# Optimization experiments

Measured on AMD Instinct MI355X. Metric: run time of the kernel, lower is better.

Reference implementation:

```python
import jax, jax.numpy as jnp
import numpy as np
from jax import lax

B, L = 16, 256
NUM_ITEMS, NUM_ATTRS = 30000, 2000
D_MODEL, D_STATE, D_CONV, N_LAYERS = 256, 16, 4, 4
D_INNER = 2 * D_MODEL
DT_RANK = (D_MODEL + 15) // 16  # ceil(d_model/16)
LN_EPS = 1e-5


def setup_inputs() -> dict:
    key = jax.random.key(0)
    ks = jax.random.split(key, 12)
    def nrm(k, shape, scale):
        return jax.random.normal(k, shape, jnp.float32) * scale
    inp = {}
    inp["seq"] = jax.random.randint(ks[0], (B, L), 0, NUM_ITEMS)
    inp["attr"] = jax.random.randint(ks[1], (B, L), 0, NUM_ATTRS)
    inp["item_emb"] = nrm(ks[2], (NUM_ITEMS, D_MODEL), 0.02)
    inp["attr_emb"] = nrm(ks[3], (NUM_ATTRS, D_MODEL), 0.02)
    inp["alpha"] = jnp.float32(0.5)
    inp["ln_s"] = jnp.ones((D_MODEL,), jnp.float32)
    inp["ln_b"] = jnp.zeros((D_MODEL,), jnp.float32)
    inp["in_w"] = nrm(ks[4], (N_LAYERS, D_MODEL, 2 * D_INNER), D_MODEL ** -0.5)
    inp["conv_w"] = nrm(ks[5], (N_LAYERS, D_INNER, 1, D_CONV), D_CONV ** -0.5)  # depthwise OIH
    inp["conv_b"] = jnp.zeros((N_LAYERS, D_INNER), jnp.float32)
    inp["xp_w"] = nrm(ks[6], (N_LAYERS, D_INNER, DT_RANK + 2 * D_STATE), D_INNER ** -0.5)
    inp["dt_w"] = nrm(ks[7], (N_LAYERS, DT_RANK, D_INNER), DT_RANK ** -0.5)
    inp["dt_b"] = jnp.zeros((N_LAYERS, D_INNER), jnp.float32)
    inp["A_log"] = jnp.tile(jnp.log(jnp.arange(1, D_STATE + 1, dtype=jnp.float32)), (N_LAYERS, D_INNER, 1))
    inp["D_p"] = jnp.ones((N_LAYERS, D_INNER), jnp.float32)
    inp["out_w"] = nrm(ks[8], (N_LAYERS, D_INNER, D_MODEL), D_INNER ** -0.5)
    inp["nrm_s"] = jnp.ones((N_LAYERS, D_MODEL), jnp.float32)
    inp["nrm_b"] = jnp.zeros((N_LAYERS, D_MODEL), jnp.float32)
    inp["head_w"] = nrm(ks[9], (D_MODEL, NUM_ITEMS), D_MODEL ** -0.5)
    return inp


def _silu(x):
    return x * jax.nn.sigmoid(x)


def _layernorm(x, s, b):
    m = jnp.mean(x, axis=-1, keepdims=True)
    v = jnp.mean(jnp.square(x - m), axis=-1, keepdims=True)
    return (x - m) * lax.rsqrt(v + LN_EPS) * s + b


def _holo_bind(x, y):
    # circular convolution via orthonormal rFFT
    xf = jnp.fft.rfft(x, axis=-1, norm="ortho")
    yf = jnp.fft.rfft(y, axis=-1, norm="ortho")
    return jnp.fft.irfft(xf * yf, n=x.shape[-1], axis=-1, norm="ortho")


def _mamba(x, in_w, conv_w, conv_b, xp_w, dt_w, dt_b, A_log, D_p, out_w):
    # x: [B, L, D_MODEL]
    xi, z = jnp.split(x @ in_w, 2, axis=-1)  # each [B, L, D_INNER]
    # causal depthwise conv (torch pads both sides then truncates to L == left pad)
    xc = lax.conv_general_dilated(
        xi.transpose(0, 2, 1), conv_w, (1,), [(D_CONV - 1, 0)],
        feature_group_count=D_INNER, dimension_numbers=("NCH", "OIH", "NCH"),
    ) + conv_b[None, :, None]
    xc = _silu(xc).transpose(0, 2, 1)  # [B, L, D_INNER]
    dt, B_ssm, C_ssm = jnp.split(xc @ xp_w, [DT_RANK, DT_RANK + D_STATE], axis=-1)
    dt = jax.nn.softplus(dt @ dt_w + dt_b)  # [B, L, D_INNER]
    A = -jnp.exp(A_log)  # [D_INNER, D_STATE]
    dA = jnp.exp(jnp.einsum("bld,dn->bldn", dt, A))
    dBx = jnp.einsum("bld,bln->bldn", dt, B_ssm) * xc[..., None]

    def step(h, inp):
        dA_t, dBx_t, C_t = inp
        h = dA_t * h + dBx_t  # [B, D_INNER, D_STATE]
        return h, jnp.einsum("bdn,bn->bd", h, C_t)

    h0 = jnp.zeros((x.shape[0], D_INNER, D_STATE), x.dtype)
    _, ys = lax.scan(step, h0, (dA.transpose(1, 0, 2, 3), dBx.transpose(1, 0, 2, 3), C_ssm.transpose(1, 0, 2)))
    y = ys.transpose(1, 0, 2) + xc * D_p
    return (y * _silu(z)) @ out_w


def reference(seq, attr, item_emb, attr_emb, alpha, ln_s, ln_b, in_w, conv_w, conv_b,
              xp_w, dt_w, dt_b, A_log, D_p, out_w, nrm_s, nrm_b, head_w):
    ie = item_emb.at[0].set(0.0)  # padding_idx=0
    ae = attr_emb.at[0].set(0.0)
    ei, ea = ie[seq], ae[attr]  # [B, L, D_MODEL]
    x = _layernorm(ei + alpha * _holo_bind(ei, ea), ln_s, ln_b)
    for l in range(N_LAYERS):
        x = x + _mamba(_layernorm(x, nrm_s[l], nrm_b[l]), in_w[l], conv_w[l], conv_b[l],
                       xp_w[l], dt_w[l], dt_b[l], A_log[l], D_p[l], out_w[l])
    return x @ head_w  # [B, L, NUM_ITEMS]
```

## Files before the change

kernel.cpp:

```cpp
#include <hip/hip_runtime.h>
#include <hip/hip_bf16.h>
#include <math.h>

#define BB 16
#define LL 256
#define DM 256
#define DI 512
#define DS 16
#define DTR 16
#define NTOK (BB*LL)
#define LN_EPS 1e-5f

typedef __attribute__((ext_vector_type(8))) short bf16x8;
typedef __attribute__((ext_vector_type(4))) float f32x4;
typedef __attribute__((ext_vector_type(4))) unsigned int u32x4;

__device__ __forceinline__ float siluf(float x) { return x / (1.f + expf(-x)); }

__device__ __forceinline__ unsigned short f2bf(float f) {
    union { float f; unsigned int u; } x; x.f = f;
    unsigned int r = x.u + 0x7fffu + ((x.u >> 16) & 1u);
    return (unsigned short)(r >> 16);
}
__device__ __forceinline__ float bf2f(unsigned short h) {
    union { unsigned int u; float f; } x; x.u = ((unsigned int)h) << 16; return x.f;
}

__device__ __forceinline__ void block_reduce2(float& s, float& s2, float* red) {
    #pragma unroll
    for (int off = 32; off; off >>= 1) {
        s  += __shfl_down(s,  off);
        s2 += __shfl_down(s2, off);
    }
    int wid = threadIdx.x >> 6;
    if ((threadIdx.x & 63) == 0) { red[wid*2] = s; red[wid*2+1] = s2; }
    __syncthreads();
    s  = red[0] + red[2] + red[4] + red[6];
    s2 = red[1] + red[3] + red[5] + red[7];
}

__global__ __launch_bounds__(256)
void embed_holo_ln(const int* __restrict__ seq, const int* __restrict__ attr,
                   const float* __restrict__ item_emb, const float* __restrict__ attr_emb,
                   const float* __restrict__ alpha_p, const float* __restrict__ ln_s,
                   const float* __restrict__ ln_b, float* __restrict__ x) {
    int t = blockIdx.x;
    int k = threadIdx.x;
    __shared__ float ei[DM], ea[DM];
    __shared__ float red[8];
    int si = seq[t], ai = attr[t];
    ei[k] = (si == 0) ? 0.f : item_emb[(size_t)si * DM + k];
    ea[k] = (ai == 0) ? 0.f : attr_emb[(size_t)ai * DM + k];
    __syncthreads();
    float c0 = 0.f, c1 = 0.f, c2 = 0.f, c3 = 0.f;
    #pragma unroll 8
    for (int j = 0; j < DM; j += 4) {
        c0 = fmaf(ei[j],   ea[(k - j)     & 255], c0);
        c1 = fmaf(ei[j+1], ea[(k - j - 1) & 255], c1);
        c2 = fmaf(ei[j+2], ea[(k - j - 2) & 255], c2);
        c3 = fmaf(ei[j+3], ea[(k - j - 3) & 255], c3);
    }
    float conv = (c0 + c1) + (c2 + c3);
    float v = fmaf(alpha_p[0] * 0.0625f, conv, ei[k]);
    float s = v, s2 = v * v;
    block_reduce2(s, s2, red);
    float m  = s * (1.f / DM);
    float var = s2 * (1.f / DM) - m * m;
    x[(size_t)t * DM + k] = (v - m) * rsqrtf(var + LN_EPS) * ln_s[k] + ln_b[k];
}

__global__ __launch_bounds__(256)
void ln_split2(const float* __restrict__ in, const float* __restrict__ sc,
               const float* __restrict__ bi, unsigned short* __restrict__ Ap) {
    int t = blockIdx.x, k = threadIdx.x;
    __shared__ float red[8];
    float v = in[(size_t)t * DM + k];
    float s = v, s2 = v * v;
    block_reduce2(s, s2, red);
    float m  = s * (1.f / DM);
    float var = s2 * (1.f / DM) - m * m;
    float o = (v - m) * rsqrtf(var + LN_EPS) * sc[k] + bi[k];
    unsigned short hi = f2bf(o);
    size_t base = (size_t)t * (2 * DM);
    Ap[base + k] = hi; Ap[base + DM + k] = hi;
}

__global__ __launch_bounds__(256)
void cvt_B2(const float* __restrict__ W, unsigned short* __restrict__ Bt, int K, int N) {
    int k0 = blockIdx.x * 64, n0 = blockIdx.y * 64;
    int K2 = 2 * K;
    __shared__ float tile[64][65];
    int tid = threadIdx.x;
    #pragma unroll
    for (int i = 0; i < 16; ++i) {
        int idx = tid + i * 256;
        int r = idx >> 6, c = idx & 63;
        int n = n0 + c;
        tile[r][c] = (n < N) ? W[(size_t)(k0 + r) * N + n] : 0.f;
    }
    __syncthreads();
    int nn = tid >> 2, kb = (tid & 3) * 16;
    alignas(16) unsigned short hv[16], lv[16];
    #pragma unroll
    for (int j = 0; j < 16; ++j) {
        float v = tile[kb + j][nn];
        hv[j] = f2bf(v); lv[j] = f2bf(v - bf2f(hv[j]));
    }
    size_t base = (size_t)(n0 + nn) * K2 + k0 + kb;
    *(u32x4*)&Bt[base]         = *(u32x4*)&hv[0];
    *(u32x4*)&Bt[base + 8]     = *(u32x4*)&hv[8];
    *(u32x4*)&Bt[base + K]     = *(u32x4*)&lv[0];
    *(u32x4*)&Bt[base + K + 8] = *(u32x4*)&lv[8];
}

__global__ __launch_bounds__(256)
void cvt_B3(const float* __restrict__ W, unsigned short* __restrict__ Bt, int K, int N) {
    int k0 = blockIdx.x * 64, n0 = blockIdx.y * 64;
    int K3 = 3 * K;
    __shared__ float tile[64][65];
    int tid = threadIdx.x;
    #pragma unroll
    for (int i = 0; i < 16; ++i) {
        int idx = tid + i * 256;
        int r = idx >> 6, c = idx & 63;
        int n = n0 + c;
        tile[r][c] = (n < N) ? W[(size_t)(k0 + r) * N + n] : 0.f;
    }
    __syncthreads();
    int nn = tid >> 2, kb = (tid & 3) * 16;
    alignas(16) unsigned short hv[16], lv[16];
    #pragma unroll
    for (int j = 0; j < 16; ++j) {
        float v = tile[kb + j][nn];
        hv[j] = f2bf(v); lv[j] = f2bf(v - bf2f(hv[j]));
    }
    size_t base = (size_t)(n0 + nn) * K3 + k0 + kb;
    *(u32x4*)&Bt[base]           = *(u32x4*)&hv[0];
    *(u32x4*)&Bt[base + 8]       = *(u32x4*)&hv[8];
    *(u32x4*)&Bt[base + K]       = *(u32x4*)&lv[0];
    *(u32x4*)&Bt[base + K + 8]   = *(u32x4*)&lv[8];
    *(u32x4*)&Bt[base + 2*K]     = *(u32x4*)&hv[0];
    *(u32x4*)&Bt[base + 2*K + 8] = *(u32x4*)&hv[8];
}

__global__ __launch_bounds__(256)
void cvt_A3(const float* __restrict__ X, unsigned short* __restrict__ Ap) {
    int i = blockIdx.x * 256 + threadIdx.x;
    int t = i >> 5, kc = (i & 31) * 8;
    const float4* X4 = (const float4*)X;
    float4 v0 = X4[(size_t)i * 2], v1 = X4[(size_t)i * 2 + 1];
    float vv[8] = { v0.x, v0.y, v0.z, v0.w, v1.x, v1.y, v1.z, v1.w };
    alignas(16) unsigned short hv[8], lv[8];
    #pragma unroll
    for (int j = 0; j < 8; ++j) { hv[j] = f2bf(vv[j]); lv[j] = f2bf(vv[j] - bf2f(hv[j])); }
    size_t base = (size_t)t * 768 + kc;
    *(u32x4*)&Ap[base]       = *(u32x4*)&hv[0];
    *(u32x4*)&Ap[base + 256] = *(u32x4*)&hv[0];
    *(u32x4*)&Ap[base + 512] = *(u32x4*)&lv[0];
}

template<bool ACC, bool SWZ>
__global__ __launch_bounds__(256)
void gemm_bf16t(const unsigned short* __restrict__ A, const unsigned short* __restrict__ Bt,
                float* __restrict__ C, int N, int K) {
    __shared__ unsigned short sA[128 * 32];
    __shared__ unsigned short sB[128 * 32];
    int tid = threadIdx.x, lane = tid & 63, w = tid >> 6;
    int wr = w >> 1, wc = w & 1;
    int row0, col0;
    if (SWZ) {
        int nwg = gridDim.x * gridDim.y;
        int chunk = nwg >> 3;
        int bid = blockIdx.y * gridDim.x + blockIdx.x;
        int idx = (bid & 7) * chunk + (bid >> 3);
        int rowt = idx % gridDim.y;
        int colt = idx / gridDim.y;
        row0 = rowt * 128; col0 = colt * 128;
    } else {
        row0 = blockIdx.y * 128; col0 = blockIdx.x * 128;
    }
    f32x4 acc[4][4] = {};
    int rA = lane >> 2;
    int kc = (lane & 3) * 8;
    for (int k0 = 0; k0 < K; k0 += 32) {
        #pragma unroll
        for (int i = 0; i < 2; ++i) {
            int rr = (w * 2 + i) * 16 + rA;
            const unsigned short* ga = A  + (size_t)(row0 + rr) * K + k0 + kc;
            const unsigned short* gb = Bt + (size_t)(col0 + rr) * K + k0 + kc;
            __builtin_amdgcn_global_load_lds(
                (const __attribute__((address_space(1))) unsigned int*)ga,
                (__attribute__((address_space(3))) unsigned int*)(sA + (w * 2 + i) * 512), 16, 0, 0);
            __builtin_amdgcn_global_load_lds(
                (const __attribute__((address_space(1))) unsigned int*)gb,
                (__attribute__((address_space(3))) unsigned int*)(sB + (w * 2 + i) * 512), 16, 0, 0);
        }
        __syncthreads();
        bf16x8 av[4], bv[4];
        #pragma unroll
        for (int m = 0; m < 4; ++m)
            av[m] = *(const bf16x8*)(sA + (wr * 64 + m * 16 + (lane & 15)) * 32 + (lane >> 4) * 8);
        #pragma unroll
        for (int n = 0; n < 4; ++n)
            bv[n] = *(const bf16x8*)(sB + (wc * 64 + n * 16 + (lane & 15)) * 32 + (lane >> 4) * 8);
        #pragma unroll
        for (int m = 0; m < 4; ++m)
            #pragma unroll
            for (int n = 0; n < 4; ++n)
                acc[m][n] = __builtin_amdgcn_mfma_f32_16x16x32_bf16(av[m], bv[n], acc[m][n], 0, 0, 0);
        __syncthreads();
    }
    #pragma unroll
    for (int m = 0; m < 4; ++m) {
        int rg = row0 + wr * 64 + m * 16 + (lane >> 4) * 4;
        #pragma unroll
        for (int n = 0; n < 4; ++n) {
            int cg = col0 + wc * 64 + n * 16 + (lane & 15);
            if (cg < N) {
                float* p = C + (size_t)rg * N + cg;
                #pragma unroll
                for (int r = 0; r < 4; ++r) {
                    if (ACC)      p[(size_t)r * N] += acc[m][n][r];
                    else if (SWZ) __builtin_nontemporal_store(acc[m][n][r], p + (size_t)r * N);
                    else          p[(size_t)r * N]  = acc[m][n][r];
                }
            }
        }
    }
}

__global__ __launch_bounds__(256)
void conv_silu(const float* __restrict__ xz, const float* __restrict__ w,
               const float* __restrict__ cb, float* __restrict__ xc,
               unsigned short* __restrict__ Xc3) {
    int t = blockIdx.x;
    int d = (blockIdx.y << 8) + threadIdx.x;
    int l = t & (LL - 1);
    float acc = cb[d];
    #pragma unroll
    for (int tt = 0; tt < 4; ++tt) {
        int ls = l - 3 + tt;
        if (ls >= 0) acc = fmaf(xz[(size_t)(t - 3 + tt) * (2 * DI) + d], w[d * 4 + tt], acc);
    }
    float v = siluf(acc);
    xc[(size_t)t * DI + d] = v;
    unsigned short hi = f2bf(v), lo = f2bf(v - bf2f(hi));
    size_t base = (size_t)t * (3 * DI);
    Xc3[base + d] = hi; Xc3[base + DI + d] = hi; Xc3[base + 2 * DI + d] = lo;
}

#define NCH 4
#define TCH 64
__global__ __launch_bounds__(256)
void scan_p1(const float* __restrict__ dtbc, const float* __restrict__ xc,
             const float* __restrict__ dt_w, const float* __restrict__ dt_b,
             const float* __restrict__ A_log, const float* __restrict__ D_p,
             float* __restrict__ y, float* __restrict__ Hend, float* __restrict__ Pb) {
    int d = blockIdx.x * 256 + threadIdx.x;
    int b = blockIdx.y, c = blockIdx.z;
    int t0 = b * LL + c * TCH;
    __shared__ float rs[TCH * 48];
    const float* src = dtbc + (size_t)t0 * 48;
    #pragma unroll
    for (int i = 0; i < 12; ++i) rs[threadIdx.x + i * 256] = src[threadIdx.x + i * 256];
    __syncthreads();
    float Av[DS], h[DS], P[DS], Wd[DTR];
    #pragma unroll
    for (int n = 0; n < DS; ++n) { Av[n] = -expf(A_log[d * DS + n]); h[n] = 0.f; P[n] = 1.f; }
    #pragma unroll
    for (int k = 0; k < DTR; ++k) Wd[k] = dt_w[k * DI + d];
    float bias = dt_b[d], Dv = D_p[d];
    for (int t = 0; t < TCH; ++t) {
        const float* r = rs + t * 48;
        float s = bias;
        #pragma unroll
        for (int k = 0; k < DTR; ++k) s = fmaf(r[k], Wd[k], s);
        float dt = (s > 20.f) ? s : log1pf(expf(s));
        float xv = xc[(size_t)(t0 + t) * DI + d];
        float dtx = dt * xv, acc = 0.f;
        #pragma unroll
        for (int n = 0; n < DS; ++n) {
            float dA = expf(dt * Av[n]);
            h[n] = fmaf(dA, h[n], dtx * r[DTR + n]);
            P[n] *= dA;
            acc = fmaf(h[n], r[DTR + DS + n], acc);
        }
        y[(size_t)(t0 + t) * DI + d] = fmaf(xv, Dv, acc);
    }
    size_t sb = ((size_t)(b * NCH + c) * DI + d) * DS;
    #pragma unroll
    for (int n = 0; n < DS; ++n) { Hend[sb + n] = h[n]; Pb[sb + n] = P[n]; }
}

__global__ __launch_bounds__(256)
void scan_p2(const float* __restrict__ dtbc,
             const float* __restrict__ dt_w, const float* __restrict__ dt_b,
             const float* __restrict__ A_log,
             float* __restrict__ y, const float* __restrict__ Hend,
             const float* __restrict__ Pb) {
    int d = blockIdx.x * 256 + threadIdx.x;
    int b = blockIdx.y, c = blockIdx.z + 1;
    int t0 = b * LL + c * TCH;
    __shared__ float rs[TCH * 48];
    const float* src = dtbc + (size_t)t0 * 48;
    #pragma unroll
    for (int i = 0; i < 12; ++i) rs[threadIdx.x + i * 256] = src[threadIdx.x + i * 256];
    __syncthreads();
    float Av[DS], g[DS], Wd[DTR];
    #pragma unroll
    for (int n = 0; n < DS; ++n) Av[n] = -expf(A_log[d * DS + n]);
    #pragma unroll
    for (int k = 0; k < DTR; ++k) Wd[k] = dt_w[k * DI + d];
    float bias = dt_b[d];
    {
        size_t sb0 = ((size_t)(b * NCH + 0) * DI + d) * DS;
        #pragma unroll
        for (int n = 0; n < DS; ++n) g[n] = Hend[sb0 + n];
        for (int cc = 1; cc < c; ++cc) {
            size_t sb = ((size_t)(b * NCH + cc) * DI + d) * DS;
            #pragma unroll
            for (int n = 0; n < DS; ++n) g[n] = fmaf(Pb[sb + n], g[n], Hend[sb + n]);
        }
    }
    for (int t = 0; t < TCH; ++t) {
        const float* r = rs + t * 48;
        float s = bias;
        #pragma unroll
        for (int k = 0; k < DTR; ++k) s = fmaf(r[k], Wd[k], s);
        float dt = (s > 20.f) ? s : log1pf(expf(s));
        float acc = 0.f;
        #pragma unroll
        for (int n = 0; n < DS; ++n) {
            g[n] *= expf(dt * Av[n]);
            acc = fmaf(g[n], r[DTR + DS + n], acc);
        }
        size_t yi = (size_t)(t0 + t) * DI + d;
        y[yi] += acc;
    }
}

__global__ __launch_bounds__(256)
void gate_split2(const float* __restrict__ xz, const float* __restrict__ y,
                 unsigned short* __restrict__ Yp) {
    int i = blockIdx.x * 256 + threadIdx.x;
    int t = i >> 9, d = i & (DI - 1);
    float g = y[i] * siluf(xz[(size_t)t * (2 * DI) + DI + d]);
    unsigned short hi = f2bf(g);
    size_t base = (size_t)t * (2 * DI);
    Yp[base + d] = hi; Yp[base + DI + d] = hi;
}

extern "C" void kernel_launch(void* const* d_in, const int* in_sizes, int n_in,
                              void* d_out, int out_size, void* d_ws, size_t ws_size,
                              hipStream_t stream) {
    const int*   seq      = (const int*)d_in[0];
    const int*   attr     = (const int*)d_in[1];
    const float* item_emb = (const float*)d_in[2];
    const float* attr_emb = (const float*)d_in[3];
    const float* alpha    = (const float*)d_in[4];
    const float* ln_s     = (const float*)d_in[5];
    const float* ln_b     = (const float*)d_in[6];
    const float* in_w     = (const float*)d_in[7];
    const float* conv_w   = (const float*)d_in[8];
    const float* conv_b   = (const float*)d_in[9];
    const float* xp_w     = (const float*)d_in[10];
    const float* dt_w     = (const float*)d_in[11];
    const float* dt_b     = (const float*)d_in[12];
    const float* A_log    = (const float*)d_in[13];
    const float* D_p      = (const float*)d_in[14];
    const float* out_w    = (const float*)d_in[15];
    const float* nrm_s    = (const float*)d_in[16];
    const float* nrm_b    = (const float*)d_in[17];
    const float* head_w   = (const float*)d_in[18];
    float* out = (float*)d_out;

    char* w8 = (char*)d_ws;
    float*          x     = (float*)(w8);
    unsigned short* Ap    = (unsigned short*)(w8 +  4194304);
    float*          Hend  = (float*)(w8 +  4194304);
    float*          Pb    = (float*)(w8 +  6291456);
    float*          xz    = (float*)(w8 +  8388608);
    float*          xc    = (float*)(w8 + 25165824);
    unsigned short* Xc3   = (unsigned short*)(w8 + 33554432);
    unsigned short* Yp    = (unsigned short*)(w8 + 33554432);
    float*          yb    = (float*)(w8 + 46137344);
    float*          dtbc  = (float*)(w8 + 54525952);
    unsigned short* Btin  = (unsigned short*)(w8 + 55312384);
    unsigned short* Btxp  = (unsigned short*)(w8 + 56360960);
    unsigned short* Btout = (unsigned short*)(w8 + 56754176);
    unsigned short* Ap3   = (unsigned short*)(w8 +  4194304);
    unsigned short* Bth   = (unsigned short*)(w8 + 10485760);

    embed_holo_ln<<<NTOK, 256, 0, stream>>>(seq, attr, item_emb, attr_emb, alpha, ln_s, ln_b, x);

    for (int l = 0; l < 4; ++l) {
        ln_split2<<<NTOK, 256, 0, stream>>>(x, nrm_s + l * DM, nrm_b + l * DM, Ap);
        cvt_B2<<<dim3(4, 16), 256, 0, stream>>>(in_w + (size_t)l * DM * 1024, Btin, DM, 1024);
        gemm_bf16t<false, false><<<dim3(8, 32), 256, 0, stream>>>(Ap, Btin, xz, 1024, 2 * DM);
        conv_silu<<<dim3(NTOK, 2), 256, 0, stream>>>(
            xz, conv_w + (size_t)l * DI * 4, conv_b + (size_t)l * DI, xc, Xc3);
        cvt_B3<<<dim3(8, 2), 256, 0, stream>>>(xp_w + (size_t)l * DI * 48, Btxp, DI, 48);
        gemm_bf16t<false, false><<<dim3(1, 32), 256, 0, stream>>>(Xc3, Btxp, dtbc, 48, 3 * DI);
        scan_p1<<<dim3(2, BB, NCH), 256, 0, stream>>>(
            dtbc, xc, dt_w + (size_t)l * DTR * DI, dt_b + (size_t)l * DI,
            A_log + (size_t)l * DI * DS, D_p + (size_t)l * DI, yb, Hend, Pb);
        scan_p2<<<dim3(2, BB, NCH - 1), 256, 0, stream>>>(
            dtbc, dt_w + (size_t)l * DTR * DI, dt_b + (size_t)l * DI,
            A_log + (size_t)l * DI * DS, yb, Hend, Pb);
        gate_split2<<<(NTOK * DI) / 256, 256, 0, stream>>>(xz, yb, Yp);
        cvt_B2<<<dim3(8, 4), 256, 0, stream>>>(out_w + (size_t)l * DI * DM, Btout, DI, DM);
        gemm_bf16t<true, false><<<dim3(2, 32), 256, 0, stream>>>(Yp, Btout, x, DM, 2 * DI);
    }

    cvt_A3<<<(NTOK * DM / 8) / 256, 256, 0, stream>>>(x, Ap3);
    cvt_B3<<<dim3(4, 470), 256, 0, stream>>>(head_w, Bth, DM, 30000);
    gemm_bf16t<false, true><<<dim3(235, 32), 256, 0, stream>>>(Ap3, Bth, out, 30000, 3 * DM);
}
```

Measured before the change: 1.914 ms.

## Merge prep kernels, fuse gating into scan, shorten scan chunks, stage head stores

Combines LayerNorm and the three weight conversions of each layer into one launch, and the head A/B conversions into another, to cut launch count. Folds the SiLU gate and bf16 split into both scan passes, which removes the separate gate kernel and a full read of y. Scan chunks change from 4x64 to 8x32 for more parallelism, at the cost of more carry-propagation work in pass 2. The head GEMM epilogue is staged through shared memory so it can issue vectorized nontemporal 16-byte stores, which adds extra barriers.

```diff
diff --git a/kernel.cpp b/kernel.cpp
--- a/kernel.cpp
+++ b/kernel.cpp
@@ -10,6 +10,8 @@
 #define DTR 16
 #define NTOK (BB*LL)
 #define LN_EPS 1e-5f
+#define NCH 8
+#define TCH 32
 
 typedef __attribute__((ext_vector_type(8))) short bf16x8;
 typedef __attribute__((ext_vector_type(4))) float f32x4;
@@ -37,6 +39,62 @@
     __syncthreads();
     s  = red[0] + red[2] + red[4] + red[6];
     s2 = red[1] + red[3] + red[5] + red[7];
+}
+
+__device__ __forceinline__ void cvtB2_body(const float* __restrict__ W, unsigned short* __restrict__ Bt,
+                                           int K, int N, int bkx, int bny, float* tile) {
+    int k0 = bkx * 64, n0 = bny * 64;
+    int K2 = 2 * K;
+    int tid = threadIdx.x;
+    #pragma unroll
+    for (int i = 0; i < 16; ++i) {
+        int idx = tid + i * 256;
+        int r = idx >> 6, c = idx & 63;
+        int n = n0 + c;
+        tile[r * 65 + c] = (n < N) ? W[(size_t)(k0 + r) * N + n] : 0.f;
+    }
+    __syncthreads();
+    int nn = tid >> 2, kb = (tid & 3) * 16;
+    alignas(16) unsigned short hv[16], lv[16];
+    #pragma unroll
+    for (int j = 0; j < 16; ++j) {
+        float v = tile[(kb + j) * 65 + nn];
+        hv[j] = f2bf(v); lv[j] = f2bf(v - bf2f(hv[j]));
+    }
+    size_t base = (size_t)(n0 + nn) * K2 + k0 + kb;
+    *(u32x4*)&Bt[base]         = *(u32x4*)&hv[0];
+    *(u32x4*)&Bt[base + 8]     = *(u32x4*)&hv[8];
+    *(u32x4*)&Bt[base + K]     = *(u32x4*)&lv[0];
+    *(u32x4*)&Bt[base + K + 8] = *(u32x4*)&lv[8];
+}
+
+__device__ __forceinline__ void cvtB3_body(const float* __restrict__ W, unsigned short* __restrict__ Bt,
+                                           int K, int N, int bkx, int bny, float* tile) {
+    int k0 = bkx * 64, n0 = bny * 64;
+    int K3 = 3 * K;
+    int tid = threadIdx.x;
+    #pragma unroll
+    for (int i = 0; i < 16; ++i) {
+        int idx = tid + i * 256;
+        int r = idx >> 6, c = idx & 63;
+        int n = n0 + c;
+        tile[r * 65 + c] = (n < N) ? W[(size_t)(k0 + r) * N + n] : 0.f;
+    }
+    __syncthreads();
+    int nn = tid >> 2, kb = (tid & 3) * 16;
+    alignas(16) unsigned short hv[16], lv[16];
+    #pragma unroll
+    for (int j = 0; j < 16; ++j) {
+        float v = tile[(kb + j) * 65 + nn];
+        hv[j] = f2bf(v); lv[j] = f2bf(v - bf2f(hv[j]));
+    }
+    size_t base = (size_t)(n0 + nn) * K3 + k0 + kb;
+    *(u32x4*)&Bt[base]           = *(u32x4*)&hv[0];
+    *(u32x4*)&Bt[base + 8]       = *(u32x4*)&hv[8];
+    *(u32x4*)&Bt[base + K]       = *(u32x4*)&lv[0];
+    *(u32x4*)&Bt[base + K + 8]   = *(u32x4*)&lv[8];
+    *(u32x4*)&Bt[base + 2*K]     = *(u32x4*)&hv[0];
+    *(u32x4*)&Bt[base + 2*K + 8] = *(u32x4*)&hv[8];
 }
 
 __global__ __launch_bounds__(256)
@@ -70,93 +128,58 @@
 }
 
 __global__ __launch_bounds__(256)
-void ln_split2(const float* __restrict__ in, const float* __restrict__ sc,
-               const float* __restrict__ bi, unsigned short* __restrict__ Ap) {
-    int t = blockIdx.x, k = threadIdx.x;
-    __shared__ float red[8];
-    float v = in[(size_t)t * DM + k];
-    float s = v, s2 = v * v;
-    block_reduce2(s, s2, red);
-    float m  = s * (1.f / DM);
-    float var = s2 * (1.f / DM) - m * m;
-    float o = (v - m) * rsqrtf(var + LN_EPS) * sc[k] + bi[k];
-    unsigned short hi = f2bf(o);
-    size_t base = (size_t)t * (2 * DM);
-    Ap[base + k] = hi; Ap[base + DM + k] = hi;
-}
-
-__global__ __launch_bounds__(256)
-void cvt_B2(const float* __restrict__ W, unsigned short* __restrict__ Bt, int K, int N) {
-    int k0 = blockIdx.x * 64, n0 = blockIdx.y * 64;
-    int K2 = 2 * K;
-    __shared__ float tile[64][65];
-    int tid = threadIdx.x;
-    #pragma unroll
-    for (int i = 0; i < 16; ++i) {
-        int idx = tid + i * 256;
-        int r = idx >> 6, c = idx & 63;
-        int n = n0 + c;
-        tile[r][c] = (n < N) ? W[(size_t)(k0 + r) * N + n] : 0.f;
-    }
-    __syncthreads();
-    int nn = tid >> 2, kb = (tid & 3) * 16;
-    alignas(16) unsigned short hv[16], lv[16];
-    #pragma unroll
-    for (int j = 0; j < 16; ++j) {
-        float v = tile[kb + j][nn];
-        hv[j] = f2bf(v); lv[j] = f2bf(v - bf2f(hv[j]));
-    }
-    size_t base = (size_t)(n0 + nn) * K2 + k0 + kb;
-    *(u32x4*)&Bt[base]         = *(u32x4*)&hv[0];
-    *(u32x4*)&Bt[base + 8]     = *(u32x4*)&hv[8];
-    *(u32x4*)&Bt[base + K]     = *(u32x4*)&lv[0];
-    *(u32x4*)&Bt[base + K + 8] = *(u32x4*)&lv[8];
-}
-
-__global__ __launch_bounds__(256)
-void cvt_B3(const float* __restrict__ W, unsigned short* __restrict__ Bt, int K, int N) {
-    int k0 = blockIdx.x * 64, n0 = blockIdx.y * 64;
-    int K3 = 3 * K;
-    __shared__ float tile[64][65];
-    int tid = threadIdx.x;
-    #pragma unroll
-    for (int i = 0; i < 16; ++i) {
-        int idx = tid + i * 256;
-        int r = idx >> 6, c = idx & 63;
-        int n = n0 + c;
-        tile[r][c] = (n < N) ? W[(size_t)(k0 + r) * N + n] : 0.f;
-    }
-    __syncthreads();
-    int nn = tid >> 2, kb = (tid & 3) * 16;
-    alignas(16) unsigned short hv[16], lv[16];
-    #pragma unroll
-    for (int j = 0; j < 16; ++j) {
-        float v = tile[kb + j][nn];
-        hv[j] = f2bf(v); lv[j] = f2bf(v - bf2f(hv[j]));
-    }
-    size_t base = (size_t)(n0 + nn) * K3 + k0 + kb;
-    *(u32x4*)&Bt[base]           = *(u32x4*)&hv[0];
-    *(u32x4*)&Bt[base + 8]       = *(u32x4*)&hv[8];
-    *(u32x4*)&Bt[base + K]       = *(u32x4*)&lv[0];
-    *(u32x4*)&Bt[base + K + 8]   = *(u32x4*)&lv[8];
-    *(u32x4*)&Bt[base + 2*K]     = *(u32x4*)&hv[0];
-    *(u32x4*)&Bt[base + 2*K + 8] = *(u32x4*)&hv[8];
-}
-
-__global__ __launch_bounds__(256)
-void cvt_A3(const float* __restrict__ X, unsigned short* __restrict__ Ap) {
-    int i = blockIdx.x * 256 + threadIdx.x;
-    int t = i >> 5, kc = (i & 31) * 8;
-    const float4* X4 = (const float4*)X;
-    float4 v0 = X4[(size_t)i * 2], v1 = X4[(size_t)i * 2 + 1];
-    float vv[8] = { v0.x, v0.y, v0.z, v0.w, v1.x, v1.y, v1.z, v1.w };
-    alignas(16) unsigned short hv[8], lv[8];
-    #pragma unroll
-    for (int j = 0; j < 8; ++j) { hv[j] = f2bf(vv[j]); lv[j] = f2bf(vv[j] - bf2f(hv[j])); }
-    size_t base = (size_t)t * 768 + kc;
-    *(u32x4*)&Ap[base]       = *(u32x4*)&hv[0];
-    *(u32x4*)&Ap[base + 256] = *(u32x4*)&hv[0];
-    *(u32x4*)&Ap[base + 512] = *(u32x4*)&lv[0];
+void layer_prep(const float* __restrict__ x, const float* __restrict__ sc,
+                const float* __restrict__ bi, unsigned short* __restrict__ Ap,
+                const float* __restrict__ in_w_l, unsigned short* __restrict__ Btin,
+                const float* __restrict__ xp_w_l, unsigned short* __restrict__ Btxp,
+                const float* __restrict__ out_w_l, unsigned short* __restrict__ Btout) {
+    __shared__ float sh[64 * 65];
+    int bid = blockIdx.x;
+    if (bid < NTOK) {
+        int t = bid, k = threadIdx.x;
+        float v = x[(size_t)t * DM + k];
+        float s = v, s2 = v * v;
+        block_reduce2(s, s2, sh);
+        float m  = s * (1.f / DM);
+        float var = s2 * (1.f / DM) - m * m;
+        float o = (v - m) * rsqrtf(var + LN_EPS) * sc[k] + bi[k];
+        unsigned short hi = f2bf(o);
+        size_t base = (size_t)t * (2 * DM);
+        Ap[base + k] = hi; Ap[base + DM + k] = hi;
+    } else if (bid < NTOK + 64) {
+        int idx = bid - NTOK;
+        cvtB2_body(in_w_l, Btin, DM, 1024, idx & 3, idx >> 2, sh);
+    } else if (bid < NTOK + 80) {
+        int idx = bid - (NTOK + 64);
+        cvtB3_body(xp_w_l, Btxp, DI, 48, idx & 7, idx >> 3, sh);
+    } else {
+        int idx = bid - (NTOK + 80);
+        cvtB2_body(out_w_l, Btout, DI, DM, idx & 7, idx >> 3, sh);
+    }
+}
+
+__global__ __launch_bounds__(256)
+void head_prep(const float* __restrict__ X, unsigned short* __restrict__ Ap3,
+               const float* __restrict__ head_w, unsigned short* __restrict__ Bth) {
+    __shared__ float sh[64 * 65];
+    int bid = blockIdx.x;
+    if (bid < 512) {
+        int i = bid * 256 + threadIdx.x;
+        int t = i >> 5, kc = (i & 31) * 8;
+        const f32x4* X4 = (const f32x4*)X;
+        f32x4 v0 = X4[(size_t)i * 2], v1 = X4[(size_t)i * 2 + 1];
+        float vv[8] = { v0.x, v0.y, v0.z, v0.w, v1.x, v1.y, v1.z, v1.w };
+        alignas(16) unsigned short hv[8], lv[8];
+        #pragma unroll
+        for (int j = 0; j < 8; ++j) { hv[j] = f2bf(vv[j]); lv[j] = f2bf(vv[j] - bf2f(hv[j])); }
+        size_t base = (size_t)t * 768 + kc;
+        *(u32x4*)&Ap3[base]       = *(u32x4*)&hv[0];
+        *(u32x4*)&Ap3[base + 256] = *(u32x4*)&hv[0];
+        *(u32x4*)&Ap3[base + 512] = *(u32x4*)&lv[0];
+    } else {
+        int idx = bid - 512;
+        cvtB3_body(head_w, Bth, DM, 30000, idx & 3, idx >> 2, sh);
+    }
 }
 
 template<bool ACC, bool SWZ>
@@ -210,19 +233,43 @@
                 acc[m][n] = __builtin_amdgcn_mfma_f32_16x16x32_bf16(av[m], bv[n], acc[m][n], 0, 0, 0);
         __syncthreads();
     }
-    #pragma unroll
-    for (int m = 0; m < 4; ++m) {
-        int rg = row0 + wr * 64 + m * 16 + (lane >> 4) * 4;
-        #pragma unroll
-        for (int n = 0; n < 4; ++n) {
-            int cg = col0 + wc * 64 + n * 16 + (lane & 15);
-            if (cg < N) {
-                float* p = C + (size_t)rg * N + cg;
+    if constexpr (SWZ) {
+        __shared__ float stg[4][16][68];
+        #pragma unroll
+        for (int m = 0; m < 4; ++m) {
+            #pragma unroll
+            for (int n = 0; n < 4; ++n)
                 #pragma unroll
-                for (int r = 0; r < 4; ++r) {
-                    if (ACC)      p[(size_t)r * N] += acc[m][n][r];
-                    else if (SWZ) __builtin_nontemporal_store(acc[m][n][r], p + (size_t)r * N);
-                    else          p[(size_t)r * N]  = acc[m][n][r];
+                for (int r = 0; r < 4; ++r)
+                    stg[w][(lane >> 4) * 4 + r][n * 16 + (lane & 15)] = acc[m][n][r];
+            __syncthreads();
+            int rsub = lane >> 4;
+            int c4   = (lane & 15) * 4;
+            #pragma unroll
+            for (int rg4 = 0; rg4 < 4; ++rg4) {
+                int rr = rg4 * 4 + rsub;
+                int rg = row0 + wr * 64 + m * 16 + rr;
+                int cg = col0 + wc * 64 + c4;
+                if (cg < N)
+                    __builtin_nontemporal_store(*(const f32x4*)&stg[w][rr][c4],
+                                                (f32x4*)(C + (size_t)rg * N + cg));
+            }
+            __syncthreads();
+        }
+    } else {
+        #pragma unroll
+        for (int m = 0; m < 4; ++m) {
+            int rg = row0 + wr * 64 + m * 16 + (lane >> 4) * 4;
+            #pragma unroll
+            for (int n = 0; n < 4; ++n) {
+                int cg = col0 + wc * 64 + n * 16 + (lane & 15);
+                if (cg < N) {
+                    float* p = C + (size_t)rg * N + cg;
+                    #pragma unroll
+                    for (int r = 0; r < 4; ++r) {
+                        if (ACC) p[(size_t)r * N] += acc[m][n][r];
+                        else     p[(size_t)r * N]  = acc[m][n][r];
+                    }
                 }
             }
         }
@@ -249,20 +296,20 @@
     Xc3[base + d] = hi; Xc3[base + DI + d] = hi; Xc3[base + 2 * DI + d] = lo;
 }
 
-#define NCH 4
-#define TCH 64
 __global__ __launch_bounds__(256)
 void scan_p1(const float* __restrict__ dtbc, const float* __restrict__ xc,
+             const float* __restrict__ xz,
              const float* __restrict__ dt_w, const float* __restrict__ dt_b,
              const float* __restrict__ A_log, const float* __restrict__ D_p,
-             float* __restrict__ y, float* __restrict__ Hend, float* __restrict__ Pb) {
+             float* __restrict__ y, float* __restrict__ Hend, float* __restrict__ Pb,
+             unsigned short* __restrict__ Yp) {
     int d = blockIdx.x * 256 + threadIdx.x;
     int b = blockIdx.y, c = blockIdx.z;
     int t0 = b * LL + c * TCH;
     __shared__ float rs[TCH * 48];
     const float* src = dtbc + (size_t)t0 * 48;
     #pragma unroll
-    for (int i = 0; i < 12; ++i) rs[threadIdx.x + i * 256] = src[threadIdx.x + i * 256];
+    for (int i = 0; i < 6; ++i) rs[threadIdx.x + i * 256] = src[threadIdx.x + i * 256];
     __syncthreads();
     float Av[DS], h[DS], P[DS], Wd[DTR];
     #pragma unroll
@@ -285,7 +332,16 @@
             P[n] *= dA;
             acc = fmaf(h[n], r[DTR + DS + n], acc);
         }
-        y[(size_t)(t0 + t) * DI + d] = fmaf(xv, Dv, acc);
+        float yv = fmaf(xv, Dv, acc);
+        if (c == 0) {
+            float z = xz[(size_t)(t0 + t) * (2 * DI) + DI + d];
+            float g = yv * siluf(z);
+            unsigned short hi = f2bf(g);
+            size_t base = (size_t)(t0 + t) * (2 * DI);
+            Yp[base + d] = hi; Yp[base + DI + d] = hi;
+        } else {
+            y[(size_t)(t0 + t) * DI + d] = yv;
+        }
     }
     size_t sb = ((size_t)(b * NCH + c) * DI + d) * DS;
     #pragma unroll
@@ -293,18 +349,18 @@
 }
 
 __global__ __launch_bounds__(256)
-void scan_p2(const float* __restrict__ dtbc,
+void scan_p2(const float* __restrict__ dtbc, const float* __restrict__ xz,
              const float* __restrict__ dt_w, const float* __restrict__ dt_b,
              const float* __restrict__ A_log,
-             float* __restrict__ y, const float* __restrict__ Hend,
-             const float* __restrict__ Pb) {
+             const float* __restrict__ y, const float* __restrict__ Hend,
+             const float* __restrict__ Pb, unsigned short* __restrict__ Yp) {
     int d = blockIdx.x * 256 + threadIdx.x;
     int b = blockIdx.y, c = blockIdx.z + 1;
     int t0 = b * LL + c * TCH;
     __shared__ float rs[TCH * 48];
     const float* src = dtbc + (size_t)t0 * 48;
     #pragma unroll
-    for (int i = 0; i < 12; ++i) rs[threadIdx.x + i * 256] = src[threadIdx.x + i * 256];
+    for (int i = 0; i < 6; ++i) rs[threadIdx.x + i * 256] = src[threadIdx.x + i * 256];
     __syncthreads();
     float Av[DS], g[DS], Wd[DTR];
     #pragma unroll
@@ -334,20 +390,13 @@
             g[n] *= expf(dt * Av[n]);
             acc = fmaf(g[n], r[DTR + DS + n], acc);
         }
-        size_t yi = (size_t)(t0 + t) * DI + d;
-        y[yi] += acc;
-    }
-}
-
-__global__ __launch_bounds__(256)
-void gate_split2(const float* __restrict__ xz, const float* __restrict__ y,
-                 unsigned short* __restrict__ Yp) {
-    int i = blockIdx.x * 256 + threadIdx.x;
-    int t = i >> 9, d = i & (DI - 1);
-    float g = y[i] * siluf(xz[(size_t)t * (2 * DI) + DI + d]);
-    unsigned short hi = f2bf(g);
-    size_t base = (size_t)t * (2 * DI);
-    Yp[base + d] = hi; Yp[base + DI + d] = hi;
+        float yv = y[(size_t)(t0 + t) * DI + d] + acc;
+        float z = xz[(size_t)(t0 + t) * (2 * DI) + DI + d];
+        float gg = yv * siluf(z);
+        unsigned short hi = f2bf(gg);
+        size_t base = (size_t)(t0 + t) * (2 * DI);
+        Yp[base + d] = hi; Yp[base + DI + d] = hi;
+    }
 }
 
 extern "C" void kernel_launch(void* const* d_in, const int* in_sizes, int n_in,
@@ -377,12 +426,12 @@
     char* w8 = (char*)d_ws;
     float*          x     = (float*)(w8);
     unsigned short* Ap    = (unsigned short*)(w8 +  4194304);
-    float*          Hend  = (float*)(w8 +  4194304);
-    float*          Pb    = (float*)(w8 +  6291456);
+    float*          Pb    = (float*)(w8 +  4194304);
     float*          xz    = (float*)(w8 +  8388608);
     float*          xc    = (float*)(w8 + 25165824);
     unsigned short* Xc3   = (unsigned short*)(w8 + 33554432);
     unsigned short* Yp    = (unsigned short*)(w8 + 33554432);
+    float*          Hend  = (float*)(w8 + 41943040);
     float*          yb    = (float*)(w8 + 46137344);
     float*          dtbc  = (float*)(w8 + 54525952);
     unsigned short* Btin  = (unsigned short*)(w8 + 55312384);
@@ -394,25 +443,24 @@
     embed_holo_ln<<<NTOK, 256, 0, stream>>>(seq, attr, item_emb, attr_emb, alpha, ln_s, ln_b, x);
 
     for (int l = 0; l < 4; ++l) {
-        ln_split2<<<NTOK, 256, 0, stream>>>(x, nrm_s + l * DM, nrm_b + l * DM, Ap);
-        cvt_B2<<<dim3(4, 16), 256, 0, stream>>>(in_w + (size_t)l * DM * 1024, Btin, DM, 1024);
+        layer_prep<<<NTOK + 112, 256, 0, stream>>>(
+            x, nrm_s + l * DM, nrm_b + l * DM, Ap,
+            in_w + (size_t)l * DM * 1024, Btin,
+            xp_w + (size_t)l * DI * 48, Btxp,
+            out_w + (size_t)l * DI * DM, Btout);
         gemm_bf16t<false, false><<<dim3(8, 32), 256, 0, stream>>>(Ap, Btin, xz, 1024, 2 * DM);
         conv_silu<<<dim3(NTOK, 2), 256, 0, stream>>>(
             xz, conv_w + (size_t)l * DI * 4, conv_b + (size_t)l * DI, xc, Xc3);
-        cvt_B3<<<dim3(8, 2), 256, 0, stream>>>(xp_w + (size_t)l * DI * 48, Btxp, DI, 48);
         gemm_bf16t<false, false><<<dim3(1, 32), 256, 0, stream>>>(Xc3, Btxp, dtbc, 48, 3 * DI);
         scan_p1<<<dim3(2, BB, NCH), 256, 0, stream>>>(
-            dtbc, xc, dt_w + (size_t)l * DTR * DI, dt_b + (size_t)l * DI,
-            A_log + (size_t)l * DI * DS, D_p + (size_t)l * DI, yb, Hend, Pb);
+            dtbc, xc, xz, dt_w + (size_t)l * DTR * DI, dt_b + (size_t)l * DI,
+            A_log + (size_t)l * DI * DS, D_p + (size_t)l * DI, yb, Hend, Pb, Yp);
         scan_p2<<<dim3(2, BB, NCH - 1), 256, 0, stream>>>(
-            dtbc, dt_w + (size_t)l * DTR * DI, dt_b + (size_t)l * DI,
-            A_log + (size_t)l * DI * DS, yb, Hend, Pb);
-        gate_split2<<<(NTOK * DI) / 256, 256, 0, stream>>>(xz, yb, Yp);
-        cvt_B2<<<dim3(8, 4), 256, 0, stream>>>(out_w + (size_t)l * DI * DM, Btout, DI, DM);
+            dtbc, xz, dt_w + (size_t)l * DTR * DI, dt_b + (size_t)l * DI,
+            A_log + (size_t)l * DI * DS, yb, Hend, Pb, Yp);
         gemm_bf16t<true, false><<<dim3(2, 32), 256, 0, stream>>>(Yp, Btout, x, DM, 2 * DI);
     }
 
-    cvt_A3<<<(NTOK * DM / 8) / 256, 256, 0, stream>>>(x, Ap3);
-    cvt_B3<<<dim3(4, 470), 256, 0, stream>>>(head_w, Bth, DM, 30000);
+    head_prep<<<512 + 1880, 256, 0, stream>>>(x, Ap3, head_w, Bth);
     gemm_bf16t<false, true><<<dim3(235, 32), 256, 0, stream>>>(Ap3, Bth, out, 30000, 3 * DM);
 }
```

Result: faster. 1.605 ms (-16.1%).
